# Kernel tuning notes

Hardware: AMD Instinct MI355X
Metric: run time of the kernel (lower is better)

Reference implementation:

```python
import jax, jax.numpy as jnp
import numpy as np

B, T, E, H = 1, 2048, 2048, 32
D = E // H  # head_dim = 64


def alibi_bias(n_heads, t_q, t_k, dtype):
    # slopes: 2^(-8*(h+1)/n_heads) for power-of-two head counts
    slopes = jnp.power(2.0, -8.0 * jnp.arange(1, n_heads + 1, dtype=jnp.float32) / n_heads)
    i = jnp.arange(t_q)[:, None] + (t_k - t_q)  # absolute query positions
    j = jnp.arange(t_k)[None, :]
    rel = (j - i).astype(dtype)                 # [t_q, t_k], <=0 on/below diagonal
    return (slopes[:, None, None] * rel).astype(dtype)  # [H, t_q, t_k]


def setup_inputs() -> dict:
    key = jax.random.key(0)
    kx, kq, kk, kv, ko = jax.random.split(key, 5)
    s = E ** -0.5
    x = jax.random.normal(kx, (B, T, E), dtype=jnp.float32)
    Wq = jax.random.normal(kq, (E, E), dtype=jnp.float32) * s
    Wk = jax.random.normal(kk, (D, E), dtype=jnp.float32) * s
    Wv = jax.random.normal(kv, (D, E), dtype=jnp.float32) * s
    Wo = jax.random.normal(ko, (E, E), dtype=jnp.float32) * s
    # causal mask: True where attention is disallowed (j > i)
    attention_mask = jnp.triu(jnp.ones((T, T), dtype=bool), k=1)[None, None]  # [1,1,T,T]
    return {"x": x, "Wq": Wq, "Wk": Wk, "Wv": Wv, "Wo": Wo, "attention_mask": attention_mask}


def reference(x, Wq, Wk, Wv, Wo, attention_mask):
    b, t, _ = x.shape
    scale = D ** -0.5
    q = (x @ Wq.T).reshape(b, t, H, D).transpose(0, 2, 1, 3)  # [b,H,t,D]
    k = x @ Wk.T                                              # [b,t,D] (single KV head)
    v = x @ Wv.T                                              # [b,t,D]
    attn = jnp.einsum('bhtd,bsd->bhts', q * scale, k)         # [b,H,t,t]
    attn = attn + alibi_bias(H, t, t, attn.dtype)[None]
    attn = jnp.where(attention_mask, jnp.asarray(-10000.0, attn.dtype), attn)
    w = jax.nn.softmax(attn, axis=-1)
    out = jnp.einsum('bhts,bsd->bhtd', w, v)                  # [b,H,t,D]
    out = out.transpose(0, 2, 1, 3).reshape(b, t, E)
    return out @ Wo.T
```

## Files before the change

### kernel.cpp

```cpp
#include <hip/hip_runtime.h>
#include <stdint.h>
#include <math.h>

typedef __bf16 bf16;
typedef __bf16 bf16x4 __attribute__((ext_vector_type(4)));
typedef __bf16 bf16x8 __attribute__((ext_vector_type(8)));
typedef short short4v __attribute__((ext_vector_type(4)));
typedef float floatx4 __attribute__((ext_vector_type(4)));

#define MFMA32(a, b, c) __builtin_amdgcn_mfma_f32_16x16x32_bf16((a), (b), (c), 0, 0, 0)

__device__ __forceinline__ floatx4 mfma16(bf16x4 a, bf16x4 b, floatx4 c) {
  return __builtin_amdgcn_mfma_f32_16x16x16bf16_1k(
      __builtin_bit_cast(short4v, a), __builtin_bit_cast(short4v, b), c, 0, 0, 0);
}

__device__ __forceinline__ void gload16(const void* g, void* l) {
  __builtin_amdgcn_global_load_lds(
      (const __attribute__((address_space(1))) void*)g,
      (__attribute__((address_space(3))) void*)l, 16, 0, 0);
}

__device__ __forceinline__ bf16x8 load8(const float* p) {
  float4 lo = *(const float4*)p;
  float4 hi = *(const float4*)(p + 4);
  bf16x8 r;
  r[0] = (bf16)lo.x; r[1] = (bf16)lo.y; r[2] = (bf16)lo.z; r[3] = (bf16)lo.w;
  r[4] = (bf16)hi.x; r[5] = (bf16)hi.y; r[6] = (bf16)hi.z; r[7] = (bf16)hi.w;
  return r;
}

__global__ __launch_bounds__(256) void conv3(const float* __restrict__ a, bf16* __restrict__ ab,
                                             const float* __restrict__ b, bf16* __restrict__ bb,
                                             const float* __restrict__ c, bf16* __restrict__ cb) {
  const int i = blockIdx.x * 256 + threadIdx.x;
  const float* src = blockIdx.y == 0 ? a : (blockIdx.y == 1 ? b : c);
  bf16* dst = blockIdx.y == 0 ? ab : (blockIdx.y == 1 ? bb : cb);
  ((bf16x8*)dst)[i] = load8(src + (size_t)i * 8);
}

__global__ __launch_bounds__(256) void pack_kv(const float* __restrict__ Kf,
                                               const float* __restrict__ Vf,
                                               bf16* __restrict__ Kb,
                                               bf16* __restrict__ Vtb) {
  int i = blockIdx.x * 256 + threadIdx.x;
  if (i < 2048 * 64) {
    Kb[i] = (bf16)Kf[i];
    const int t = i >> 6, d = i & 63;
    Vtb[(size_t)d * 2048 + t] = (bf16)Vf[i];
  }
}

template <typename TC>
__global__ __launch_bounds__(256) void gemm_bt_a(const bf16* __restrict__ A,
                                                 const bf16* __restrict__ B,
                                                 TC* __restrict__ C,
                                                 int M, int N, int K) {
  __shared__ __align__(16) bf16 As[2][64 * 32];
  __shared__ __align__(16) bf16 Bs[2][128 * 32];
  const int tid = threadIdx.x;
  const int wave = tid >> 6, lane = tid & 63;
  const int quad = lane >> 4, l16 = lane & 15;
  const int wg = blockIdx.y * 16 + blockIdx.x;
  const int wgid = (wg & 7) * 64 + (wg >> 3);
  const int m0 = (wgid >> 4) * 64, n0 = (wgid & 15) * 128;
  const int wm = (wave >> 1) * 32, wn = (wave & 1) * 64;

  floatx4 acc[2][4];
#pragma unroll
  for (int i = 0; i < 2; i++)
#pragma unroll
    for (int j = 0; j < 4; j++) acc[i][j] = (floatx4)0.f;

  const int srow = tid >> 2;
  const int scol = ((tid & 3) ^ ((tid >> 3) & 3)) * 8;
  const bf16* Ap = A + (size_t)(m0 + srow) * K + scol;
  const bf16* Bp = B + (size_t)(n0 + srow) * K + scol;

  auto stage = [&](int k0, int buf) {
    gload16(Ap + k0, (char*)As[buf] + tid * 16);
    gload16(Bp + k0, (char*)Bs[buf] + tid * 16);
    gload16(Bp + (size_t)64 * K + k0, (char*)Bs[buf] + 4096 + tid * 16);
  };
  const int sxg = (l16 >> 1) & 3;
  auto compute = [&](int buf) {
    bf16x8 af[2], bfr[4];
#pragma unroll
    for (int mt = 0; mt < 2; mt++)
      af[mt] = *(const bf16x8*)(&As[buf][(wm + mt * 16 + l16) * 32 + ((quad ^ sxg) * 8)]);
#pragma unroll
    for (int nt = 0; nt < 4; nt++)
      bfr[nt] = *(const bf16x8*)(&Bs[buf][(wn + nt * 16 + l16) * 32 + ((quad ^ sxg) * 8)]);
#pragma unroll
    for (int mt = 0; mt < 2; mt++)
#pragma unroll
      for (int nt = 0; nt < 4; nt++)
        acc[mt][nt] = MFMA32(af[mt], bfr[nt], acc[mt][nt]);
  };

  stage(0, 0);
  for (int k0 = 0; k0 < K; k0 += 64) {
    __syncthreads();
    if (k0 + 32 < K) stage(k0 + 32, 1);
    compute(0);
    __syncthreads();
    if (k0 + 64 < K) stage(k0 + 64, 0);
    compute(1);
  }

#pragma unroll
  for (int mt = 0; mt < 2; mt++) {
#pragma unroll
    for (int nt = 0; nt < 4; nt++) {
      const int col = n0 + wn + nt * 16 + l16;
      const int row = m0 + wm + mt * 16 + quad * 4;
#pragma unroll
      for (int r = 0; r < 4; r++)
        C[(size_t)(row + r) * N + col] = (TC)acc[mt][nt][r];
    }
  }
}

__global__ __launch_bounds__(256) void kv_gemm(const bf16* __restrict__ xb,
                                               const float* __restrict__ Wk,
                                               const float* __restrict__ Wv,
                                               float* __restrict__ Kf,
                                               float* __restrict__ Vf) {
  __shared__ __align__(16) bf16 As[128 * 40];
  __shared__ __align__(16) bf16 Bs[128 * 40];
  const int tid = threadIdx.x;
  const int wave = tid >> 6, lane = tid & 63;
  const int quad = lane >> 4, l16 = lane & 15;
  const int m0 = blockIdx.y * 128;
  const int kbeg = blockIdx.x * 256, kend = kbeg + 256;
  const int wm = (wave >> 1) * 64, wn = (wave & 1) * 64;

  floatx4 acc[4][4];
#pragma unroll
  for (int i = 0; i < 4; i++)
#pragma unroll
    for (int j = 0; j < 4; j++) acc[i][j] = (floatx4)0.f;

  const int sr = tid >> 2, sc = (tid & 3) * 8;

  for (int k0 = kbeg; k0 < kend; k0 += 32) {
    __syncthreads();
#pragma unroll
    for (int rr = 0; rr < 2; rr++) {
      const int row = sr + rr * 64;
      *(bf16x8*)(&As[row * 40 + sc]) =
          *(const bf16x8*)(&xb[(size_t)(m0 + row) * 2048 + k0 + sc]);
      const float* bsrc = (row < 64) ? &Wk[(size_t)row * 2048 + k0 + sc]
                                     : &Wv[(size_t)(row - 64) * 2048 + k0 + sc];
      *(bf16x8*)(&Bs[row * 40 + sc]) = load8(bsrc);
    }
    __syncthreads();

    bf16x8 af[4], bfr[4];
#pragma unroll
    for (int mt = 0; mt < 4; mt++)
      af[mt] = *(const bf16x8*)(&As[(wm + mt * 16 + l16) * 40 + quad * 8]);
#pragma unroll
    for (int nt = 0; nt < 4; nt++)
      bfr[nt] = *(const bf16x8*)(&Bs[(wn + nt * 16 + l16) * 40 + quad * 8]);
#pragma unroll
    for (int mt = 0; mt < 4; mt++)
#pragma unroll
      for (int nt = 0; nt < 4; nt++)
        acc[mt][nt] = MFMA32(af[mt], bfr[nt], acc[mt][nt]);
  }

#pragma unroll
  for (int mt = 0; mt < 4; mt++) {
#pragma unroll
    for (int nt = 0; nt < 4; nt++) {
      const int col = wn + nt * 16 + l16;
      const int row = m0 + wm + mt * 16 + quad * 4;
      float* dst = (col < 64) ? &Kf[(size_t)row * 64 + col]
                              : &Vf[(size_t)row * 64 + (col - 64)];
#pragma unroll
      for (int r = 0; r < 4; r++) atomicAdd(dst + (size_t)r * 64, acc[mt][nt][r]);
    }
  }
}

#define WTHR 30.f

__global__ __launch_bounds__(1024) void mktable(uint32_t* __restrict__ tbl) {
  __shared__ int bins[17], base[17];
  const int i = threadIdx.x;
  const int p = i & 511, hf = i >> 9;
  const int h = p & 31, t = p >> 5;
  const float slope2 = exp2f(-0.25f * (float)(h + 1)) * 1.44269504f;
  const int lo_key = t * 128 - (int)(WTHR / slope2);
  const int lo_t = (lo_key <= 0) ? 0 : (lo_key >> 6);
  const int m = 2 * t + 2 - lo_t;
  const int load = hf ? (m >> 1) : ((m + 1) >> 1);
  if (i < 17) bins[i] = 0;
  __syncthreads();
  atomicAdd(&bins[load], 1);
  __syncthreads();
  if (i == 0) {
    int s = 0;
    for (int v = 16; v >= 0; --v) { base[v] = s; s += bins[v]; }
  }
  __syncthreads();
  if (i < 17) bins[i] = 0;
  __syncthreads();
  const int off = atomicAdd(&bins[load], 1);
  const int rank = base[load] + off;
  tbl[rank] = ((uint32_t)hf << 9) | (uint32_t)p;
}

__global__ __launch_bounds__(512) void attn_kernel(const bf16* __restrict__ Q,
                                                   const bf16* __restrict__ Kb,
                                                   const bf16* __restrict__ Vtb,
                                                   float* __restrict__ OpA,
                                                   float* __restrict__ OpB,
                                                   float* __restrict__ lpart,
                                                   const uint32_t* __restrict__ tbl) {
  __shared__ __align__(16) bf16 Ks[2][64 * 64];
  __shared__ __align__(16) bf16 Vt[2][64 * 64];

  const int u = blockIdx.x & 255, sfold = blockIdx.x >> 8;
  const int r = (sfold == 0) ? u : (sfold == 1) ? (511 - u)
                : (sfold == 2) ? (512 + u) : (1023 - u);
  const uint32_t e = tbl[r];
  const int p = e & 511, hf = (int)(e >> 9);
  const int h = p & 31, t = p >> 5;

  const float slope2 = exp2f(-0.25f * (float)(h + 1)) * 1.44269504f;
  const int lo_key = t * 128 - (int)(WTHR / slope2);
  const int lo_t = (lo_key <= 0) ? 0 : (lo_key >> 6);
  const int m = 2 * t + 2 - lo_t;
  const int c0 = (m + 1) >> 1;
  const int kbeg = hf ? (lo_t + c0) : lo_t;
  const int cnt = hf ? (m >> 1) : c0;

  const int tid = threadIdx.x;
  const int wave = tid >> 6;
  const int lane = tid & 63;
  const int quad = lane >> 4, l16 = lane & 15;
  const float scale2 = 0.125f * 1.44269504f;
  const bf16x4 ones = {(bf16)1.f, (bf16)1.f, (bf16)1.f, (bf16)1.f};

  float cq[4];
#pragma unroll
  for (int rr = 0; rr < 4; rr++) cq[rr] = slope2 * (float)(quad * 4 + rr);
  const float s16 = slope2 * 16.f;

  const int qi = t * 128 + wave * 16 + l16;
  const int qw0 = t * 128 + wave * 16;
  bf16x8 qf[2];
#pragma unroll
  for (int kk = 0; kk < 2; kk++)
    qf[kk] = *(const bf16x8*)(&Q[(size_t)qi * 2048 + h * 64 + kk * 32 + quad * 8]);

  floatx4 oacc[4];
#pragma unroll
  for (int dt = 0; dt < 4; dt++) oacc[dt] = (floatx4)0.f;
  floatx4 lacc = (floatx4)0.f;

  const int r0 = tid >> 3, sl = tid & 7;
  const int wsw = ((sl ^ (r0 & 7)) << 3);
  const int sx = l16 & 7;

  const int kn = kbeg * 64;
  bf16x8 kreg = *(const bf16x8*)(&Kb[(size_t)(kn + r0) * 64 + sl * 8]);
  bf16x8 vreg = *(const bf16x8*)(&Vtb[(size_t)r0 * 2048 + kn + sl * 8]);

  for (int i = 0; i < cnt; i++) {
    const int kt = kbeg + i;
    const int buf = i & 1;
    *(bf16x8*)(&Ks[buf][r0 * 64 + wsw]) = kreg;
    *(bf16x8*)(&Vt[buf][r0 * 64 + wsw]) = vreg;
    __syncthreads();
    if (i + 1 < cnt) {
      const int kn2 = (kt + 1) * 64;
      kreg = *(const bf16x8*)(&Kb[(size_t)(kn2 + r0) * 64 + sl * 8]);
      vreg = *(const bf16x8*)(&Vtb[(size_t)r0 * 2048 + kn2 + sl * 8]);
    }
    const int k0 = kt * 64;
    if (k0 > qw0 + 15) continue;
    if ((float)(qw0 - k0 - 63) * slope2 > WTHR) continue;

    const bf16* ks = Ks[buf];
    const bf16* vs = Vt[buf];

    floatx4 s[4];
#pragma unroll
    for (int mt = 0; mt < 4; mt++) s[mt] = (floatx4)0.f;
#pragma unroll
    for (int kk = 0; kk < 2; kk++) {
#pragma unroll
      for (int mt = 0; mt < 4; mt++) {
        bf16x8 kf = *(const bf16x8*)(
            &ks[(mt * 16 + l16) * 64 + (((kk * 4 + quad) ^ sx) << 3)]);
        s[mt] = MFMA32(kf, qf[kk], s[mt]);
      }
    }

    const float base0 = slope2 * (float)(k0 - qi);
    bf16x4 pb[4];
    if (k0 + 63 <= qw0) {
      float b = base0;
#pragma unroll
      for (int mt = 0; mt < 4; mt++) {
        bf16x4 tb;
#pragma unroll
        for (int rr = 0; rr < 4; rr++)
          tb[rr] = (bf16)exp2f(__builtin_fmaf(s[mt][rr], scale2, b + cq[rr]));
        pb[mt] = tb;
        b += s16;
      }
    } else {
      const int qloc = qi - k0;
      float b = base0;
#pragma unroll
      for (int mt = 0; mt < 4; mt++) {
        bf16x4 tb;
#pragma unroll
        for (int rr = 0; rr < 4; rr++) {
          const int moff = mt * 16 + quad * 4 + rr;
          const float pv = exp2f(__builtin_fmaf(s[mt][rr], scale2, b + cq[rr]));
          tb[rr] = (moff <= qloc) ? (bf16)pv : (bf16)0.f;
        }
        pb[mt] = tb;
        b += s16;
      }
    }

#pragma unroll
    for (int mt = 0; mt < 4; mt++) {
      lacc = mfma16(ones, pb[mt], lacc);
#pragma unroll
      for (int dt = 0; dt < 4; dt++) {
        const int slot = 2 * mt + (quad >> 1);
        const bf16x4 va = *(const bf16x4*)(
            &vs[(dt * 16 + l16) * 64 + ((slot ^ sx) << 3) + (quad & 1) * 4]);
        oacc[dt] = mfma16(va, pb[mt], oacc[dt]);
      }
    }
  }

  float* op = (hf ? OpB : OpA) + (size_t)qi * 2048 + h * 64;
#pragma unroll
  for (int dt = 0; dt < 4; dt++)
#pragma unroll
    for (int rr = 0; rr < 4; rr++)
      op[dt * 16 + quad * 4 + rr] = oacc[dt][rr];
  if (quad == 0) lpart[(size_t)hf * 65536 + (size_t)qi * 32 + h] = lacc[0];
}

__global__ __launch_bounds__(256) void norm_o(const float* __restrict__ P0,
                                              const float* __restrict__ P1,
                                              const float* __restrict__ L,
                                              bf16* __restrict__ AO) {
  const int idx = blockIdx.x * 256 + threadIdx.x;
  const int qi = idx >> 8;
  const int cs = (idx & 255) << 3;
  const int h = cs >> 6;
  const float l = L[(size_t)qi * 32 + h] + L[65536 + (size_t)qi * 32 + h];
  const float linv = 1.f / l;
  const float4 a0 = *(const float4*)(P0 + (size_t)qi * 2048 + cs);
  const float4 a1 = *(const float4*)(P0 + (size_t)qi * 2048 + cs + 4);
  const float4 b0 = *(const float4*)(P1 + (size_t)qi * 2048 + cs);
  const float4 b1 = *(const float4*)(P1 + (size_t)qi * 2048 + cs + 4);
  bf16x8 o;
  o[0] = (bf16)((a0.x + b0.x) * linv); o[1] = (bf16)((a0.y + b0.y) * linv);
  o[2] = (bf16)((a0.z + b0.z) * linv); o[3] = (bf16)((a0.w + b0.w) * linv);
  o[4] = (bf16)((a1.x + b1.x) * linv); o[5] = (bf16)((a1.y + b1.y) * linv);
  o[6] = (bf16)((a1.z + b1.z) * linv); o[7] = (bf16)((a1.w + b1.w) * linv);
  *(bf16x8*)(AO + (size_t)qi * 2048 + cs) = o;
}

extern "C" void kernel_launch(void* const* d_in, const int* in_sizes, int n_in,
                              void* d_out, int out_size, void* d_ws,
                              size_t ws_size, hipStream_t stream) {
  (void)in_sizes; (void)n_in; (void)out_size; (void)ws_size;
  const float* x = (const float*)d_in[0];
  const float* Wq = (const float*)d_in[1];
  const float* Wk = (const float*)d_in[2];
  const float* Wv = (const float*)d_in[3];
  const float* Wo = (const float*)d_in[4];
  float* out = (float*)d_out;

  const size_t NE = (size_t)2048 * 2048;
  bf16* xb = (bf16*)d_ws;
  bf16* Wqb = xb + NE;
  bf16* Wob = Wqb + NE;
  bf16* Qb = Wob + NE;
  float* Kf = (float*)(Qb + NE);
  float* Vf = Kf + 2048 * 64;
  bf16* Kb = (bf16*)(Vf + 2048 * 64);
  bf16* Vtb = Kb + 2048 * 64;
  float* OpA = (float*)d_ws;
  float* OpB = out;
  float* lpart = Kf;
  uint32_t* tbl = (uint32_t*)Vf;
  bf16* AO = Qb;

  (void)hipMemsetAsync(Kf, 0, 2 * 2048 * 64 * sizeof(float), stream);
  conv3<<<dim3(2048, 3), 256, 0, stream>>>(x, xb, Wq, Wqb, Wo, Wob);
  gemm_bt_a<bf16><<<dim3(16, 32), 256, 0, stream>>>(xb, Wqb, Qb, 2048, 2048, 2048);
  kv_gemm<<<dim3(8, 16), 256, 0, stream>>>(xb, Wk, Wv, Kf, Vf);
  pack_kv<<<512, 256, 0, stream>>>(Kf, Vf, Kb, Vtb);
  mktable<<<1, 1024, 0, stream>>>(tbl);
  attn_kernel<<<1024, 512, 0, stream>>>(Qb, Kb, Vtb, OpA, OpB, lpart, tbl);
  norm_o<<<2048, 256, 0, stream>>>(OpA, OpB, lpart, AO);
  gemm_bt_a<float><<<dim3(16, 32), 256, 0, stream>>>(AO, Wob, out, 2048, 2048, 2048);
}
```

Baseline: 236.7 us.

## Fuse split-KV merge and normalization into attention via last-block flag

Removes the separate norm_o kernel. Each attention block now increments a per-(head,tile) atomic counter after writing its partial output. The second block to finish reads the other half's partial O and l, normalizes, and writes bf16 AO directly. It also adds s_setprio around the MFMA sections to favor matrix work in wave scheduling. This saves a kernel launch and a full read/write pass, at the cost of extra fences and atomics and some reliance on memory-ordering correctness.

```diff
diff --git a/kernel.cpp b/kernel.cpp
--- a/kernel.cpp
+++ b/kernel.cpp
@@ -186,9 +186,11 @@
 
 #define WTHR 30.f
 
-__global__ __launch_bounds__(1024) void mktable(uint32_t* __restrict__ tbl) {
+__global__ __launch_bounds__(1024) void mktable(uint32_t* __restrict__ tbl,
+                                                uint32_t* __restrict__ flags) {
   __shared__ int bins[17], base[17];
   const int i = threadIdx.x;
+  if (i < 512) flags[i] = 0;
   const int p = i & 511, hf = i >> 9;
   const int h = p & 31, t = p >> 5;
   const float slope2 = exp2f(-0.25f * (float)(h + 1)) * 1.44269504f;
@@ -218,9 +220,12 @@
                                                    float* __restrict__ OpA,
                                                    float* __restrict__ OpB,
                                                    float* __restrict__ lpart,
+                                                   uint32_t* __restrict__ flags,
+                                                   bf16* __restrict__ AO,
                                                    const uint32_t* __restrict__ tbl) {
   __shared__ __align__(16) bf16 Ks[2][64 * 64];
   __shared__ __align__(16) bf16 Vt[2][64 * 64];
+  __shared__ int sdone;
 
   const int u = blockIdx.x & 255, sfold = blockIdx.x >> 8;
   const int r = (sfold == 0) ? u : (sfold == 1) ? (511 - u)
@@ -290,6 +295,7 @@
     floatx4 s[4];
 #pragma unroll
     for (int mt = 0; mt < 4; mt++) s[mt] = (floatx4)0.f;
+    __builtin_amdgcn_s_setprio(1);
 #pragma unroll
     for (int kk = 0; kk < 2; kk++) {
 #pragma unroll
@@ -299,6 +305,7 @@
         s[mt] = MFMA32(kf, qf[kk], s[mt]);
       }
     }
+    __builtin_amdgcn_s_setprio(0);
 
     const float base0 = slope2 * (float)(k0 - qi);
     bf16x4 pb[4];
@@ -330,6 +337,7 @@
       }
     }
 
+    __builtin_amdgcn_s_setprio(1);
 #pragma unroll
     for (int mt = 0; mt < 4; mt++) {
       lacc = mfma16(ones, pb[mt], lacc);
@@ -341,6 +349,7 @@
         oacc[dt] = mfma16(va, pb[mt], oacc[dt]);
       }
     }
+    __builtin_amdgcn_s_setprio(0);
   }
 
   float* op = (hf ? OpB : OpA) + (size_t)qi * 2048 + h * 64;
@@ -350,28 +359,27 @@
     for (int rr = 0; rr < 4; rr++)
       op[dt * 16 + quad * 4 + rr] = oacc[dt][rr];
   if (quad == 0) lpart[(size_t)hf * 65536 + (size_t)qi * 32 + h] = lacc[0];
-}
-
-__global__ __launch_bounds__(256) void norm_o(const float* __restrict__ P0,
-                                              const float* __restrict__ P1,
-                                              const float* __restrict__ L,
-                                              bf16* __restrict__ AO) {
-  const int idx = blockIdx.x * 256 + threadIdx.x;
-  const int qi = idx >> 8;
-  const int cs = (idx & 255) << 3;
-  const int h = cs >> 6;
-  const float l = L[(size_t)qi * 32 + h] + L[65536 + (size_t)qi * 32 + h];
-  const float linv = 1.f / l;
-  const float4 a0 = *(const float4*)(P0 + (size_t)qi * 2048 + cs);
-  const float4 a1 = *(const float4*)(P0 + (size_t)qi * 2048 + cs + 4);
-  const float4 b0 = *(const float4*)(P1 + (size_t)qi * 2048 + cs);
-  const float4 b1 = *(const float4*)(P1 + (size_t)qi * 2048 + cs + 4);
-  bf16x8 o;
-  o[0] = (bf16)((a0.x + b0.x) * linv); o[1] = (bf16)((a0.y + b0.y) * linv);
-  o[2] = (bf16)((a0.z + b0.z) * linv); o[3] = (bf16)((a0.w + b0.w) * linv);
-  o[4] = (bf16)((a1.x + b1.x) * linv); o[5] = (bf16)((a1.y + b1.y) * linv);
-  o[6] = (bf16)((a1.z + b1.z) * linv); o[7] = (bf16)((a1.w + b1.w) * linv);
-  *(bf16x8*)(AO + (size_t)qi * 2048 + cs) = o;
+
+  __syncthreads();
+  if (tid == 0) {
+    __threadfence();
+    sdone = (int)atomicAdd(&flags[p], 1u);
+  }
+  __syncthreads();
+  if (sdone == 1) {
+    __threadfence();
+    const float* pp = (hf ? OpA : OpB) + (size_t)qi * 2048 + h * 64;
+    const float pl = lpart[(size_t)(hf ^ 1) * 65536 + (size_t)qi * 32 + h];
+    const float linv = 1.f / (lacc[0] + pl);
+#pragma unroll
+    for (int dt = 0; dt < 4; dt++) {
+      bf16x4 ob;
+#pragma unroll
+      for (int rr = 0; rr < 4; rr++)
+        ob[rr] = (bf16)((oacc[dt][rr] + pp[dt * 16 + quad * 4 + rr]) * linv);
+      *(bf16x4*)(&AO[(size_t)qi * 2048 + h * 64 + dt * 16 + quad * 4]) = ob;
+    }
+  }
 }
 
 extern "C" void kernel_launch(void* const* d_in, const int* in_sizes, int n_in,
@@ -398,6 +406,7 @@
   float* OpB = out;
   float* lpart = Kf;
   uint32_t* tbl = (uint32_t*)Vf;
+  uint32_t* flags = tbl + 1024;
   bf16* AO = Qb;
 
   (void)hipMemsetAsync(Kf, 0, 2 * 2048 * 64 * sizeof(float), stream);
@@ -405,8 +414,7 @@
   gemm_bt_a<bf16><<<dim3(16, 32), 256, 0, stream>>>(xb, Wqb, Qb, 2048, 2048, 2048);
   kv_gemm<<<dim3(8, 16), 256, 0, stream>>>(xb, Wk, Wv, Kf, Vf);
   pack_kv<<<512, 256, 0, stream>>>(Kf, Vf, Kb, Vtb);
-  mktable<<<1, 1024, 0, stream>>>(tbl);
-  attn_kernel<<<1024, 512, 0, stream>>>(Qb, Kb, Vtb, OpA, OpB, lpart, tbl);
-  norm_o<<<2048, 256, 0, stream>>>(OpA, OpB, lpart, AO);
+  mktable<<<1, 1024, 0, stream>>>(tbl, flags);
+  attn_kernel<<<1024, 512, 0, stream>>>(Qb, Kb, Vtb, OpA, OpB, lpart, flags, AO, tbl);
   gemm_bt_a<float><<<dim3(16, 32), 256, 0, stream>>>(AO, Wob, out, 2048, 2048, 2048);
 }
```

Measured after the change: 506.0 us. 2.14x slower.
